# Optimization experiments

Measured on AMD Instinct MI355X. Metric: run time of the kernel, lower is better.

Reference implementation:

```python
import jax, jax.numpy as jnp
import numpy as np

N, E, D, H, C, L = 50000, 600000, 128, 128, 64, 3
LN_EPS = 1e-5


def setup_inputs() -> dict:
    key = jax.random.key(0)
    ks = jax.random.split(key, 6)
    x = jax.random.normal(ks[0], (N, D), jnp.float32)
    edge_index = jax.random.randint(ks[1], (2, E), 0, N, jnp.int32)
    Wg = jax.random.normal(ks[2], (L, D, H), jnp.float32) * (1.0 / np.sqrt(D))
    bg = jnp.zeros((L, H), jnp.float32)
    ln_g = jnp.ones((L, H), jnp.float32)
    ln_b = jnp.zeros((L, H), jnp.float32)
    mlp_W1 = jax.random.normal(ks[3], (D + L * H, H), jnp.float32) * (1.0 / np.sqrt(D + L * H))
    mlp_b1 = jnp.zeros((H,), jnp.float32)
    mlp_W2 = jax.random.normal(ks[4], (H, C), jnp.float32) * (1.0 / np.sqrt(H))
    mlp_b2 = jnp.zeros((C,), jnp.float32)
    return {"x": x, "edge_index": edge_index, "Wg": Wg, "bg": bg,
            "ln_g": ln_g, "ln_b": ln_b, "mlp_W1": mlp_W1, "mlp_b1": mlp_b1,
            "mlp_W2": mlp_W2, "mlp_b2": mlp_b2}


def _layer_norm(h, g, b):
    mu = jnp.mean(h, axis=-1, keepdims=True)
    var = jnp.mean((h - mu) ** 2, axis=-1, keepdims=True)
    return g * (h - mu) * jax.lax.rsqrt(var + LN_EPS) + b


def _gcn(h, W, b, src, dst, dinv):
    # GCNConv with added self-loops and symmetric normalization:
    # out = D^{-1/2} (A + I) D^{-1/2} (h W) + b
    hW = h @ W                                   # [N, H]
    coef = (dinv[src] * dinv[dst])[:, None]      # [E, 1]
    agg = jax.ops.segment_sum(hW[src] * coef, dst, num_segments=N)
    agg = agg + hW * (dinv * dinv)[:, None]      # self-loop term
    return agg + b


def reference(x, edge_index, Wg, bg, ln_g, ln_b, mlp_W1, mlp_b1, mlp_W2, mlp_b2):
    src, dst = edge_index[0], edge_index[1]
    # degree including self-loop
    deg = jnp.ones((N,), x.dtype).at[dst].add(1.0)
    dinv = jax.lax.rsqrt(deg)
    feats = [x]
    h = x
    for i in range(L):  # small fixed layer count
        h = _gcn(h, Wg[i], bg[i], src, dst, dinv)
        h = _layer_norm(h, ln_g[i], ln_b[i])
        h = jax.nn.relu(h)
        feats.append(h)
    xc = jnp.concatenate(feats, axis=1)          # [N, D + L*H]
    z = jax.nn.relu(xc @ mlp_W1 + mlp_b1)
    z = z @ mlp_W2 + mlp_b2
    return jax.nn.softmax(z, axis=1)
```

## Files before the change

### kernel.cpp

```cpp
#include <hip/hip_runtime.h>
#include <math.h>

#define D 128
#define HH 128
#define CC 64
#define NLAYERS 3
#define LN_EPS 1e-5f

typedef __attribute__((ext_vector_type(8))) short bf16x8;
typedef __attribute__((ext_vector_type(4))) float f32x4;
typedef unsigned short u16;
typedef unsigned int u32;

__device__ __forceinline__ u16 f2bf(float f) {
    u32 u = __float_as_uint(f);
    u32 r = u + 0x7FFFu + ((u >> 16) & 1u);
    return (u16)(r >> 16);
}
__device__ __forceinline__ float bf2f(u16 h) {
    return __uint_as_float(((u32)h) << 16);
}

__global__ void k_prep(const float* __restrict__ x, u16* __restrict__ xh,
                       const float* __restrict__ Wg, u16* __restrict__ WgtH,
                       const float* __restrict__ W1, u16* __restrict__ W1tH,
                       const float* __restrict__ W2, u16* __restrict__ W2tH,
                       u16* __restrict__ W2tL,
                       int* __restrict__ cnt, int N)
{
    int i = blockIdx.x * blockDim.x + threadIdx.x;
    if (i < N) { cnt[i] = 0; return; }
    i -= N;
    int nx4 = N * (D / 4);
    if (i < nx4) {
        float4 v = *(const float4*)(x + (size_t)i * 4);
        int row = i >> 5, c = (i & 31) << 2;
        ushort4 o;
        o.x = f2bf(v.x); o.y = f2bf(v.y); o.z = f2bf(v.z); o.w = f2bf(v.w);
        *(ushort4*)&xh[(size_t)row * 512 + c] = o;
        return;
    }
    i -= nx4;
    if (i < NLAYERS * D * HH) {
        int k = i >> 7, n = i & 127;
        int kc = k >> 5, q = (k >> 3) & 3, j = k & 7;
        WgtH[(((kc * 4 + q) << 7) + n) * 8 + j] = f2bf(Wg[i]);
        return;
    }
    i -= NLAYERS * D * HH;
    if (i < (D + NLAYERS * HH) * HH) {
        int k = i >> 7, n = i & 127;
        int kc = k >> 5, q = (k >> 3) & 3, j = k & 7;
        W1tH[(((kc * 4 + q) << 7) + n) * 8 + j] = f2bf(W1[i]);
        return;
    }
    i -= (D + NLAYERS * HH) * HH;
    if (i < HH * CC) {
        int k = i >> 6, n = i & 63;
        int kc = k >> 5, q = (k >> 3) & 3, j = k & 7;
        float v = W2[i];
        u16 h = f2bf(v);
        int o = (((kc * 4 + q) << 6) + n) * 8 + j;
        W2tH[o] = h;
        W2tL[o] = f2bf(v - bf2f(h));
    }
}


__global__ void k_count(const int* __restrict__ dst, int* __restrict__ cnt, int E) {
    int i = blockIdx.x * blockDim.x + threadIdx.x;
    if (i < E) atomicAdd(&cnt[dst[i]], 1);
}

__global__ void k_scan_a(const int* __restrict__ cnt, int* __restrict__ rowptr,
                         int* __restrict__ bsum, int N) {
    __shared__ int s[1024];
    int tid = threadIdx.x;
    int i = blockIdx.x * 1024 + tid;
    int v = (i < N) ? cnt[i] : 0;
    s[tid] = v;
    __syncthreads();
    for (int off = 1; off < 1024; off <<= 1) {
        int t = (tid >= off) ? s[tid - off] : 0;
        __syncthreads();
        s[tid] += t;
        __syncthreads();
    }
    if (i < N) rowptr[i] = s[tid] - v;
    if (tid == 1023) bsum[blockIdx.x] = s[tid];
}

__global__ void k_scan_c(int* __restrict__ rowptr, const int* __restrict__ bsum,
                         const int* __restrict__ cnt, float* __restrict__ dinv,
                         int* __restrict__ cursor, int N, int E, int nsb) {
    __shared__ int sb[64];
    if (threadIdx.x < 64) {
        int t = threadIdx.x;
        int v = (t < nsb) ? bsum[t] : 0;
        int incl = v;
        #pragma unroll
        for (int off = 1; off < 64; off <<= 1) {
            int u = __shfl_up(incl, off, 64);
            if (t >= off) incl += u;
        }
        sb[t] = incl - v;
    }
    __syncthreads();
    int i = blockIdx.x * blockDim.x + threadIdx.x;
    if (i < N) {
        int v = rowptr[i] + sb[i >> 10];
        rowptr[i] = v;
        cursor[i] = v;
        dinv[i] = rsqrtf(1.0f + (float)cnt[i]);
    }
    if (i == 0) rowptr[N] = E;
}

__global__ void k_scatter(const int* __restrict__ src, const int* __restrict__ dst,
                          const float* __restrict__ dinv,
                          int* __restrict__ cursor, int2* __restrict__ ecol, int E) {
    int i = blockIdx.x * blockDim.x + threadIdx.x;
    if (i < E) {
        int s = src[i], d = dst[i];
        int p = atomicAdd(&cursor[d], 1);
        float c = dinv[s] * dinv[d];
        ecol[p] = make_int2(s, __float_as_int(c));
    }
}

__global__ __launch_bounds__(256) void k_gemm_lf(
    const u16* __restrict__ A, int colOff,
    const u16* __restrict__ Bt, u16* __restrict__ OUTb, int N)
{
    const int tid  = threadIdx.x;
    const int lane = tid & 63;
    const int wave = tid >> 6;
    const int wr   = wave & 1;
    const int wc   = wave >> 1;
    const int quad = lane >> 4;
    const int l15  = lane & 15;
    const int row0 = blockIdx.x * 64;

    const u16* pA[2];
    #pragma unroll
    for (int i = 0; i < 2; ++i) {
        int r = row0 + wr * 32 + i * 16 + l15;
        if (r >= N) r = N - 1;
        pA[i] = A + (size_t)r * 512 + colOff + quad * 8;
    }
    const u16* pB = Bt + ((size_t)quad * 128 + wc * 64 + l15) * 8;

    bf16x8 ah[4][2], bh[4][4];
    #pragma unroll
    for (int kc = 0; kc < 4; ++kc) {
        #pragma unroll
        for (int i = 0; i < 2; ++i)
            ah[kc][i] = *(const bf16x8*)(pA[i] + kc * 32);
        #pragma unroll
        for (int j = 0; j < 4; ++j)
            bh[kc][j] = *(const bf16x8*)(pB + (size_t)kc * 4096 + j * 128);
    }

    f32x4 acc[2][4];
    #pragma unroll
    for (int i = 0; i < 2; ++i)
        #pragma unroll
        for (int j = 0; j < 4; ++j)
            #pragma unroll
            for (int r = 0; r < 4; ++r) acc[i][j][r] = 0.f;

    #pragma unroll
    for (int kc = 0; kc < 4; ++kc)
        #pragma unroll
        for (int i = 0; i < 2; ++i)
            #pragma unroll
            for (int j = 0; j < 4; ++j)
                acc[i][j] = __builtin_amdgcn_mfma_f32_16x16x32_bf16(ah[kc][i], bh[kc][j], acc[i][j], 0, 0, 0);

    #pragma unroll
    for (int i = 0; i < 2; ++i)
        #pragma unroll
        for (int j = 0; j < 4; ++j) {
            int col = wc * 64 + j * 16 + l15;
            #pragma unroll
            for (int r = 0; r < 4; ++r) {
                int grow = row0 + wr * 32 + i * 16 + quad * 4 + r;
                if (grow < N)
                    OUTb[(size_t)grow * 128 + col] = f2bf(acc[i][j][r]);
            }
        }
}

__global__ __launch_bounds__(256) void k_mlp_fused(
    const u16* __restrict__ xcH,
    const u16* __restrict__ B1t, const float* __restrict__ b1,
    const u16* __restrict__ W2h, const u16* __restrict__ W2l,
    const float* __restrict__ b2, float* __restrict__ out, int N)
{
    __shared__ float sAcc[32 * 132];
    __shared__ u16 sZh[32 * 128];
    __shared__ u16 sZl[32 * 128];

    const int tid  = threadIdx.x;
    const int lane = tid & 63;
    const int wave = tid >> 6;
    const int wc   = wave & 1;
    const int kg   = wave >> 1;
    const int quad = lane >> 4;
    const int l15  = lane & 15;
    const int row0 = blockIdx.x * 32;

    const u16* pA[2];
    #pragma unroll
    for (int f = 0; f < 2; ++f) {
        int r = row0 + f * 16 + l15;
        if (r >= N) r = N - 1;
        pA[f] = xcH + (size_t)r * 512 + quad * 8;
    }
    const u16* pB = B1t + ((size_t)quad * 128 + wc * 64 + l15) * 8;

    f32x4 acc[2][4];
    #pragma unroll
    for (int f = 0; f < 2; ++f)
        #pragma unroll
        for (int j = 0; j < 4; ++j)
            #pragma unroll
            for (int r = 0; r < 4; ++r) acc[f][j][r] = 0.f;

    bf16x8 abuf[3][2], bbuf[3][4];
    #define LOADI(t, s)                                                          \
        {                                                                        \
            const int g = kg * 8 + (t);                                          \
            _Pragma("unroll")                                                    \
            for (int f = 0; f < 2; ++f)                                          \
                abuf[s][f] = *(const bf16x8*)(pA[f] + g * 32);                   \
            _Pragma("unroll")                                                    \
            for (int j = 0; j < 4; ++j)                                          \
                bbuf[s][j] = *(const bf16x8*)(pB + (size_t)g * 4096 + j * 128);  \
        }
    LOADI(0, 0)
    LOADI(1, 1)
    #pragma unroll
    for (int t = 0; t < 8; ++t) {
        if (t + 2 < 8) {
            const int s = (t + 2) % 3;
            LOADI(t + 2, s)
        }
        const int u = t % 3;
        #pragma unroll
        for (int f = 0; f < 2; ++f)
            #pragma unroll
            for (int j = 0; j < 4; ++j)
                acc[f][j] = __builtin_amdgcn_mfma_f32_16x16x32_bf16(abuf[u][f], bbuf[u][j], acc[f][j], 0, 0, 0);
    }
    #undef LOADI

    if (kg == 1) {
        #pragma unroll
        for (int f = 0; f < 2; ++f)
            #pragma unroll
            for (int jt = 0; jt < 4; ++jt) {
                int col = wc * 64 + jt * 16 + l15;
                #pragma unroll
                for (int r = 0; r < 4; ++r) {
                    int row = f * 16 + quad * 4 + r;
                    sAcc[row * 132 + col] = acc[f][jt][r];
                }
            }
    }
    __syncthreads();
    if (kg == 0) {
        #pragma unroll
        for (int jt = 0; jt < 4; ++jt) {
            int col = wc * 64 + jt * 16 + l15;
            float bv = b1[col];
            int qq = col >> 3, jj = col & 7;
            #pragma unroll
            for (int f = 0; f < 2; ++f) {
                #pragma unroll
                for (int rr = 0; rr < 4; ++rr) {
                    int row = f * 16 + quad * 4 + rr;
                    float v = fmaxf(acc[f][jt][rr] + sAcc[row * 132 + col] + bv, 0.f);
                    u16 h = f2bf(v);
                    sZh[(qq * 32 + row) * 8 + jj] = h;
                    sZl[(qq * 32 + row) * 8 + jj] = f2bf(v - bf2f(h));
                }
            }
        }
    }
    __syncthreads();

    if (kg == 0) {
        f32x4 oacc[4];
        #pragma unroll
        for (int j = 0; j < 4; ++j)
            #pragma unroll
            for (int r = 0; r < 4; ++r) oacc[j][r] = 0.f;

        #pragma unroll
        for (int kc = 0; kc < 4; ++kc) {
            int qq = kc * 4 + quad;
            bf16x8 zh = *(const bf16x8*)&sZh[(qq * 32 + wc * 16 + l15) * 8];
            bf16x8 zl = *(const bf16x8*)&sZl[(qq * 32 + wc * 16 + l15) * 8];
            #pragma unroll
            for (int jt = 0; jt < 4; ++jt) {
                int n = jt * 16 + l15;
                bf16x8 wh = *(const bf16x8*)&W2h[(qq * 64 + n) * 8];
                bf16x8 wl = *(const bf16x8*)&W2l[(qq * 64 + n) * 8];
                oacc[jt] = __builtin_amdgcn_mfma_f32_16x16x32_bf16(zh, wh, oacc[jt], 0, 0, 0);
                oacc[jt] = __builtin_amdgcn_mfma_f32_16x16x32_bf16(zh, wl, oacc[jt], 0, 0, 0);
                oacc[jt] = __builtin_amdgcn_mfma_f32_16x16x32_bf16(zl, wh, oacc[jt], 0, 0, 0);
            }
        }

        #pragma unroll
        for (int jt = 0; jt < 4; ++jt) {
            float bv = b2[jt * 16 + l15];
            #pragma unroll
            for (int r = 0; r < 4; ++r) oacc[jt][r] += bv;
        }
        #pragma unroll
        for (int r = 0; r < 4; ++r) {
            float m = fmaxf(fmaxf(oacc[0][r], oacc[1][r]), fmaxf(oacc[2][r], oacc[3][r]));
            #pragma unroll
            for (int mask = 8; mask; mask >>= 1) m = fmaxf(m, __shfl_xor(m, mask, 64));
            float p0 = __expf(oacc[0][r] - m);
            float p1 = __expf(oacc[1][r] - m);
            float p2 = __expf(oacc[2][r] - m);
            float p3 = __expf(oacc[3][r] - m);
            float s = p0 + p1 + p2 + p3;
            #pragma unroll
            for (int mask = 8; mask; mask >>= 1) s += __shfl_xor(s, mask, 64);
            float inv = 1.0f / s;
            int grow = row0 + wc * 16 + quad * 4 + r;
            if (grow < N) {
                float* o = out + (size_t)grow * CC + l15;
                o[0]  = p0 * inv;
                o[16] = p1 * inv;
                o[32] = p2 * inv;
                o[48] = p3 * inv;
            }
        }
    }
}

__global__ __launch_bounds__(256, 8) void k_agg_ln(
    const u16* __restrict__ hWb,
    const int* __restrict__ rowptr, const int2* __restrict__ ecol,
    const float* __restrict__ dinv,
    const float* __restrict__ bg, const float* __restrict__ g,
    const float* __restrict__ b,
    u16* __restrict__ outHi, int N)
{
    const int lane = threadIdx.x & 63;
    const int h    = lane >> 5;
    const int c0   = (lane & 31) << 2;

    const float4 bgv = *(const float4*)(bg + c0);
    const float4 gv  = *(const float4*)(g + c0);
    const float4 bv  = *(const float4*)(b + c0);

    const int nwaves = gridDim.x * 4;
    for (int wid = blockIdx.x * 4 + (threadIdx.x >> 6); wid < N; wid += nwaves) {
        float di = dinv[wid];
        float sc = (h == 0) ? di * di : 0.f;

        uint2 hv = *(const uint2*)(hWb + (size_t)wid * HH + c0);
        float a0 = bf2f((u16)hv.x) * sc;
        float a1 = bf2f((u16)(hv.x >> 16)) * sc;
        float a2 = bf2f((u16)hv.y) * sc;
        float a3 = bf2f((u16)(hv.y >> 16)) * sc;
        float q0 = 0.f, q1 = 0.f, q2 = 0.f, q3 = 0.f;

        int e0 = rowptr[wid];
        int m  = rowptr[wid + 1] - e0;
        int ch = (m - h + 1) >> 1;
        const int2* ep = ecol + e0 + h;

        int k = 0;
        for (; k + 4 <= ch; k += 4) {
            int2 p[4];
            uint2 v[4];
            #pragma unroll
            for (int t = 0; t < 4; ++t) p[t] = ep[2 * (k + t)];
            #pragma unroll
            for (int t = 0; t < 4; ++t)
                v[t] = *(const uint2*)(hWb + (size_t)p[t].x * HH + c0);
            #pragma unroll
            for (int t = 0; t < 4; ++t) {
                float c = __int_as_float(p[t].y);
                float x0 = bf2f((u16)v[t].x) * c;
                float x1 = bf2f((u16)(v[t].x >> 16)) * c;
                float x2 = bf2f((u16)v[t].y) * c;
                float x3 = bf2f((u16)(v[t].y >> 16)) * c;
                if (t & 1) { q0 += x0; q1 += x1; q2 += x2; q3 += x3; }
                else       { a0 += x0; a1 += x1; a2 += x2; a3 += x3; }
            }
        }
        for (; k < ch; ++k) {
            int2 p = ep[2 * k];
            uint2 v = *(const uint2*)(hWb + (size_t)p.x * HH + c0);
            float c = __int_as_float(p.y);
            a0 += bf2f((u16)v.x) * c;
            a1 += bf2f((u16)(v.x >> 16)) * c;
            a2 += bf2f((u16)v.y) * c;
            a3 += bf2f((u16)(v.y >> 16)) * c;
        }
        a0 += q0; a1 += q1; a2 += q2; a3 += q3;

        a0 += __shfl_xor(a0, 32, 64);
        a1 += __shfl_xor(a1, 32, 64);
        a2 += __shfl_xor(a2, 32, 64);
        a3 += __shfl_xor(a3, 32, 64);
        a0 += bgv.x; a1 += bgv.y; a2 += bgv.z; a3 += bgv.w;

        float ssum = (a0 + a1) + (a2 + a3);
        #pragma unroll
        for (int off = 16; off; off >>= 1) ssum += __shfl_xor(ssum, off, 64);
        float mu = ssum * (1.0f / 128.0f);
        float d0 = a0 - mu, d1 = a1 - mu, d2 = a2 - mu, d3 = a3 - mu;
        float vsum = (d0 * d0 + d1 * d1) + (d2 * d2 + d3 * d3);
        #pragma unroll
        for (int off = 16; off; off >>= 1) vsum += __shfl_xor(vsum, off, 64);
        float rstd = rsqrtf(vsum * (1.0f / 128.0f) + LN_EPS);

        if (!h) {
            float o0 = fmaxf(gv.x * d0 * rstd + bv.x, 0.f);
            float o1 = fmaxf(gv.y * d1 * rstd + bv.y, 0.f);
            float o2 = fmaxf(gv.z * d2 * rstd + bv.z, 0.f);
            float o3 = fmaxf(gv.w * d3 * rstd + bv.w, 0.f);
            uint2 o;
            o.x = (u32)f2bf(o0) | ((u32)f2bf(o1) << 16);
            o.y = (u32)f2bf(o2) | ((u32)f2bf(o3) << 16);
            *(uint2*)&outHi[(size_t)wid * 512 + c0] = o;
        }
    }
}

extern "C" void kernel_launch(void* const* d_in, const int* in_sizes, int n_in,
                              void* d_out, int out_size, void* d_ws, size_t ws_size,
                              hipStream_t stream) {
    const float* x   = (const float*)d_in[0];
    const int*   ei  = (const int*)  d_in[1];
    const float* Wg  = (const float*)d_in[2];
    const float* bg  = (const float*)d_in[3];
    const float* lng = (const float*)d_in[4];
    const float* lnb = (const float*)d_in[5];
    const float* W1  = (const float*)d_in[6];
    const float* b1  = (const float*)d_in[7];
    const float* W2  = (const float*)d_in[8];
    const float* b2  = (const float*)d_in[9];
    float* out = (float*)d_out;

    const int N = in_sizes[0] / D;
    const int E = in_sizes[1] / 2;
    const int* srcp = ei;
    const int* dstp = ei + E;

    char* ws = (char*)d_ws;
    size_t off = 0;
    auto alloc = [&](size_t bytes) -> void* {
        void* p = ws + off;
        off += (bytes + 511) & ~(size_t)511;
        return p;
    };
    int*   cnt    = (int*)  alloc((size_t)N * 4);
    int*   rowptr = (int*)  alloc((size_t)(N + 1) * 4);
    int*   cursor = (int*)  alloc((size_t)N * 4);
    int*   bsum   = (int*)  alloc(64 * 4);
    int2*  ecol   = (int2*) alloc((size_t)E * 8);
    float* dinv   = (float*)alloc((size_t)N * 4);
    u16*   hWb    = (u16*)  alloc((size_t)N * HH * 2);
    u16*   xcH    = (u16*)  alloc((size_t)N * 512 * 2);
    u16*   WgtH   = (u16*)  alloc((size_t)NLAYERS * D * HH * 2);
    u16*   W1tH   = (u16*)  alloc((size_t)(D + NLAYERS * HH) * HH * 2);
    u16*   W2tH   = (u16*)  alloc((size_t)HH * CC * 2);
    u16*   W2tL   = (u16*)  alloc((size_t)HH * CC * 2);

    const int B = 256;
    const int gE = (E + B - 1) / B;
    const int nsb = (N + 1023) / 1024;

    const int prepTotal = N + N * (D / 4) + NLAYERS * D * HH
                        + (D + NLAYERS * HH) * HH + HH * CC;
    k_prep<<<(prepTotal + B - 1) / B, B, 0, stream>>>(x, xcH, Wg, WgtH, W1, W1tH,
                                                      W2, W2tH, W2tL, cnt, N);
    k_count<<<gE, B, 0, stream>>>(dstp, cnt, E);
    k_scan_a<<<nsb, 1024, 0, stream>>>(cnt, rowptr, bsum, N);
    k_scan_c<<<(N + B - 1) / B, B, 0, stream>>>(rowptr, bsum, cnt, dinv, cursor, N, E, nsb);
    k_scatter<<<gE, B, 0, stream>>>(srcp, dstp, dinv, cursor, ecol, E);

    const int gemmBlocks = (N + 63) / 64;
    const int mlpBlocks  = (N + 31) / 32;
    const int aggBlocks  = 2048;

    for (int l = 0; l < NLAYERS; ++l) {
        k_gemm_lf<<<gemmBlocks, B, 0, stream>>>(xcH, l * HH,
                                                WgtH + (size_t)l * D * HH, hWb, N);
        k_agg_ln<<<aggBlocks, B, 0, stream>>>(hWb, rowptr, ecol, dinv,
                                              bg + (size_t)l * HH,
                                              lng + (size_t)l * HH,
                                              lnb + (size_t)l * HH,
                                              xcH + (size_t)(l + 1) * HH, N);
    }

    k_mlp_fused<<<mlpBlocks, B, 0, stream>>>(xcH, W1tH, b1,
                                             W2tH, W2tL, b2, out, N);
}
```

Before: 321.7 us.

## Split aggregation wave into four edge streams with 16-byte row gathers

The aggregation+LayerNorm kernel now splits each 64-lane wave into four groups of 16 lanes. Each group handles every fourth edge and loads 8 bf16 features per lane with 16-byte loads, where before two halves each loaded 4 features. This gives more independent gathers in flight per node and wider memory transactions, at the cost of more cross-lane reductions and a lower unroll depth per edge stream. The block scan is also rewritten to use wavefront shuffles instead of a barrier-heavy shared-memory Hillis-Steele loop.

```diff
diff --git a/kernel.cpp b/kernel.cpp
--- a/kernel.cpp
+++ b/kernel.cpp
@@ -74,20 +74,32 @@
 
 __global__ void k_scan_a(const int* __restrict__ cnt, int* __restrict__ rowptr,
                          int* __restrict__ bsum, int N) {
-    __shared__ int s[1024];
-    int tid = threadIdx.x;
+    __shared__ int ws[16];
+    int tid  = threadIdx.x;
+    int lane = tid & 63, wv = tid >> 6;
     int i = blockIdx.x * 1024 + tid;
     int v = (i < N) ? cnt[i] : 0;
-    s[tid] = v;
+    int incl = v;
+    #pragma unroll
+    for (int off = 1; off < 64; off <<= 1) {
+        int u = __shfl_up(incl, off, 64);
+        if (lane >= off) incl += u;
+    }
+    if (lane == 63) ws[wv] = incl;
     __syncthreads();
-    for (int off = 1; off < 1024; off <<= 1) {
-        int t = (tid >= off) ? s[tid - off] : 0;
-        __syncthreads();
-        s[tid] += t;
-        __syncthreads();
-    }
-    if (i < N) rowptr[i] = s[tid] - v;
-    if (tid == 1023) bsum[blockIdx.x] = s[tid];
+    if (wv == 0) {
+        int s = (lane < 16) ? ws[lane] : 0;
+        #pragma unroll
+        for (int off = 1; off < 16; off <<= 1) {
+            int u = __shfl_up(s, off, 64);
+            if (lane >= off) s += u;
+        }
+        if (lane < 16) ws[lane] = s;
+    }
+    __syncthreads();
+    int add = (wv == 0) ? 0 : ws[wv - 1];
+    if (i < N) rowptr[i] = add + incl - v;
+    if (tid == 1023) bsum[blockIdx.x] = ws[15];
 }
 
 __global__ void k_scan_c(int* __restrict__ rowptr, const int* __restrict__ bsum,
@@ -353,86 +365,98 @@
     u16* __restrict__ outHi, int N)
 {
     const int lane = threadIdx.x & 63;
-    const int h    = lane >> 5;
-    const int c0   = (lane & 31) << 2;
-
-    const float4 bgv = *(const float4*)(bg + c0);
-    const float4 gv  = *(const float4*)(g + c0);
-    const float4 bv  = *(const float4*)(b + c0);
+    const int qd   = lane >> 4;
+    const int c0   = (lane & 15) << 3;
+
+    const float4 bgA = *(const float4*)(bg + c0);
+    const float4 bgB = *(const float4*)(bg + c0 + 4);
 
     const int nwaves = gridDim.x * 4;
     for (int wid = blockIdx.x * 4 + (threadIdx.x >> 6); wid < N; wid += nwaves) {
         float di = dinv[wid];
-        float sc = (h == 0) ? di * di : 0.f;
-
-        uint2 hv = *(const uint2*)(hWb + (size_t)wid * HH + c0);
-        float a0 = bf2f((u16)hv.x) * sc;
-        float a1 = bf2f((u16)(hv.x >> 16)) * sc;
-        float a2 = bf2f((u16)hv.y) * sc;
-        float a3 = bf2f((u16)(hv.y >> 16)) * sc;
-        float q0 = 0.f, q1 = 0.f, q2 = 0.f, q3 = 0.f;
+        float sc = (qd == 0) ? di * di : 0.f;
+
+        uint4 hv = *(const uint4*)(hWb + (size_t)wid * HH + c0);
+        float a0 = bf2f((u16)hv.x) * sc, a1 = bf2f((u16)(hv.x >> 16)) * sc;
+        float a2 = bf2f((u16)hv.y) * sc, a3 = bf2f((u16)(hv.y >> 16)) * sc;
+        float a4 = bf2f((u16)hv.z) * sc, a5 = bf2f((u16)(hv.z >> 16)) * sc;
+        float a6 = bf2f((u16)hv.w) * sc, a7 = bf2f((u16)(hv.w >> 16)) * sc;
 
         int e0 = rowptr[wid];
         int m  = rowptr[wid + 1] - e0;
-        int ch = (m - h + 1) >> 1;
-        const int2* ep = ecol + e0 + h;
+        int cq = (m - qd + 3) >> 2;
+        const int2* ep = ecol + e0 + qd;
 
         int k = 0;
-        for (; k + 4 <= ch; k += 4) {
+        for (; k + 4 <= cq; k += 4) {
             int2 p[4];
-            uint2 v[4];
-            #pragma unroll
-            for (int t = 0; t < 4; ++t) p[t] = ep[2 * (k + t)];
+            uint4 v[4];
+            #pragma unroll
+            for (int t = 0; t < 4; ++t) p[t] = ep[4 * (k + t)];
             #pragma unroll
             for (int t = 0; t < 4; ++t)
-                v[t] = *(const uint2*)(hWb + (size_t)p[t].x * HH + c0);
+                v[t] = *(const uint4*)(hWb + (size_t)p[t].x * HH + c0);
             #pragma unroll
             for (int t = 0; t < 4; ++t) {
                 float c = __int_as_float(p[t].y);
-                float x0 = bf2f((u16)v[t].x) * c;
-                float x1 = bf2f((u16)(v[t].x >> 16)) * c;
-                float x2 = bf2f((u16)v[t].y) * c;
-                float x3 = bf2f((u16)(v[t].y >> 16)) * c;
-                if (t & 1) { q0 += x0; q1 += x1; q2 += x2; q3 += x3; }
-                else       { a0 += x0; a1 += x1; a2 += x2; a3 += x3; }
+                a0 += bf2f((u16)v[t].x) * c;  a1 += bf2f((u16)(v[t].x >> 16)) * c;
+                a2 += bf2f((u16)v[t].y) * c;  a3 += bf2f((u16)(v[t].y >> 16)) * c;
+                a4 += bf2f((u16)v[t].z) * c;  a5 += bf2f((u16)(v[t].z >> 16)) * c;
+                a6 += bf2f((u16)v[t].w) * c;  a7 += bf2f((u16)(v[t].w >> 16)) * c;
             }
         }
-        for (; k < ch; ++k) {
-            int2 p = ep[2 * k];
-            uint2 v = *(const uint2*)(hWb + (size_t)p.x * HH + c0);
+        for (; k < cq; ++k) {
+            int2 p = ep[4 * k];
+            uint4 v = *(const uint4*)(hWb + (size_t)p.x * HH + c0);
             float c = __int_as_float(p.y);
-            a0 += bf2f((u16)v.x) * c;
-            a1 += bf2f((u16)(v.x >> 16)) * c;
-            a2 += bf2f((u16)v.y) * c;
-            a3 += bf2f((u16)(v.y >> 16)) * c;
-        }
-        a0 += q0; a1 += q1; a2 += q2; a3 += q3;
-
-        a0 += __shfl_xor(a0, 32, 64);
-        a1 += __shfl_xor(a1, 32, 64);
-        a2 += __shfl_xor(a2, 32, 64);
-        a3 += __shfl_xor(a3, 32, 64);
-        a0 += bgv.x; a1 += bgv.y; a2 += bgv.z; a3 += bgv.w;
-
-        float ssum = (a0 + a1) + (a2 + a3);
-        #pragma unroll
-        for (int off = 16; off; off >>= 1) ssum += __shfl_xor(ssum, off, 64);
+            a0 += bf2f((u16)v.x) * c;  a1 += bf2f((u16)(v.x >> 16)) * c;
+            a2 += bf2f((u16)v.y) * c;  a3 += bf2f((u16)(v.y >> 16)) * c;
+            a4 += bf2f((u16)v.z) * c;  a5 += bf2f((u16)(v.z >> 16)) * c;
+            a6 += bf2f((u16)v.w) * c;  a7 += bf2f((u16)(v.w >> 16)) * c;
+        }
+
+        a0 += __shfl_xor(a0, 16, 64); a0 += __shfl_xor(a0, 32, 64);
+        a1 += __shfl_xor(a1, 16, 64); a1 += __shfl_xor(a1, 32, 64);
+        a2 += __shfl_xor(a2, 16, 64); a2 += __shfl_xor(a2, 32, 64);
+        a3 += __shfl_xor(a3, 16, 64); a3 += __shfl_xor(a3, 32, 64);
+        a4 += __shfl_xor(a4, 16, 64); a4 += __shfl_xor(a4, 32, 64);
+        a5 += __shfl_xor(a5, 16, 64); a5 += __shfl_xor(a5, 32, 64);
+        a6 += __shfl_xor(a6, 16, 64); a6 += __shfl_xor(a6, 32, 64);
+        a7 += __shfl_xor(a7, 16, 64); a7 += __shfl_xor(a7, 32, 64);
+        a0 += bgA.x; a1 += bgA.y; a2 += bgA.z; a3 += bgA.w;
+        a4 += bgB.x; a5 += bgB.y; a6 += bgB.z; a7 += bgB.w;
+
+        float ssum = ((a0 + a1) + (a2 + a3)) + ((a4 + a5) + (a6 + a7));
+        #pragma unroll
+        for (int off = 8; off; off >>= 1) ssum += __shfl_xor(ssum, off, 64);
         float mu = ssum * (1.0f / 128.0f);
         float d0 = a0 - mu, d1 = a1 - mu, d2 = a2 - mu, d3 = a3 - mu;
-        float vsum = (d0 * d0 + d1 * d1) + (d2 * d2 + d3 * d3);
-        #pragma unroll
-        for (int off = 16; off; off >>= 1) vsum += __shfl_xor(vsum, off, 64);
+        float d4 = a4 - mu, d5 = a5 - mu, d6 = a6 - mu, d7 = a7 - mu;
+        float vsum = ((d0 * d0 + d1 * d1) + (d2 * d2 + d3 * d3))
+                   + ((d4 * d4 + d5 * d5) + (d6 * d6 + d7 * d7));
+        #pragma unroll
+        for (int off = 8; off; off >>= 1) vsum += __shfl_xor(vsum, off, 64);
         float rstd = rsqrtf(vsum * (1.0f / 128.0f) + LN_EPS);
 
-        if (!h) {
-            float o0 = fmaxf(gv.x * d0 * rstd + bv.x, 0.f);
-            float o1 = fmaxf(gv.y * d1 * rstd + bv.y, 0.f);
-            float o2 = fmaxf(gv.z * d2 * rstd + bv.z, 0.f);
-            float o3 = fmaxf(gv.w * d3 * rstd + bv.w, 0.f);
-            uint2 o;
+        if (qd == 0) {
+            const float4 gA = *(const float4*)(g + c0);
+            const float4 gB = *(const float4*)(g + c0 + 4);
+            const float4 bA = *(const float4*)(b + c0);
+            const float4 bB = *(const float4*)(b + c0 + 4);
+            float o0 = fmaxf(gA.x * d0 * rstd + bA.x, 0.f);
+            float o1 = fmaxf(gA.y * d1 * rstd + bA.y, 0.f);
+            float o2 = fmaxf(gA.z * d2 * rstd + bA.z, 0.f);
+            float o3 = fmaxf(gA.w * d3 * rstd + bA.w, 0.f);
+            float o4 = fmaxf(gB.x * d4 * rstd + bB.x, 0.f);
+            float o5 = fmaxf(gB.y * d5 * rstd + bB.y, 0.f);
+            float o6 = fmaxf(gB.z * d6 * rstd + bB.z, 0.f);
+            float o7 = fmaxf(gB.w * d7 * rstd + bB.w, 0.f);
+            uint4 o;
             o.x = (u32)f2bf(o0) | ((u32)f2bf(o1) << 16);
             o.y = (u32)f2bf(o2) | ((u32)f2bf(o3) << 16);
-            *(uint2*)&outHi[(size_t)wid * 512 + c0] = o;
+            o.z = (u32)f2bf(o4) | ((u32)f2bf(o5) << 16);
+            o.w = (u32)f2bf(o6) | ((u32)f2bf(o7) << 16);
+            *(uint4*)&outHi[(size_t)wid * 512 + c0] = o;
         }
     }
 }
```

Measured after the change: 376.3 us. 1.17x slower.

## Map one node per half-wave in aggregation and use wave-shuffle block scan

Applied to the files above, without the earlier changes.

The aggregation kernel now assigns one node to each 32-lane half-wave instead of splitting one node's edges across two half-waves. This removes the cross-half reduction and the idle output half, and handles the edge tail with a predicated three-edge batch. The scan kernel swaps its shared-memory Hillis-Steele loop, which needed many barriers, for wave shuffle scans plus a 16-entry shared fixup. The cost is that each half-wave walks a whole edge list serially, so latency per node grows and the two nodes in a wave can diverge when their degrees differ.

```diff
diff --git a/kernel.cpp b/kernel.cpp
--- a/kernel.cpp
+++ b/kernel.cpp
@@ -74,20 +74,32 @@
 
 __global__ void k_scan_a(const int* __restrict__ cnt, int* __restrict__ rowptr,
                          int* __restrict__ bsum, int N) {
-    __shared__ int s[1024];
-    int tid = threadIdx.x;
+    __shared__ int ws[16];
+    int tid  = threadIdx.x;
+    int lane = tid & 63, wv = tid >> 6;
     int i = blockIdx.x * 1024 + tid;
     int v = (i < N) ? cnt[i] : 0;
-    s[tid] = v;
+    int incl = v;
+    #pragma unroll
+    for (int off = 1; off < 64; off <<= 1) {
+        int u = __shfl_up(incl, off, 64);
+        if (lane >= off) incl += u;
+    }
+    if (lane == 63) ws[wv] = incl;
     __syncthreads();
-    for (int off = 1; off < 1024; off <<= 1) {
-        int t = (tid >= off) ? s[tid - off] : 0;
-        __syncthreads();
-        s[tid] += t;
-        __syncthreads();
-    }
-    if (i < N) rowptr[i] = s[tid] - v;
-    if (tid == 1023) bsum[blockIdx.x] = s[tid];
+    if (wv == 0) {
+        int s = (lane < 16) ? ws[lane] : 0;
+        #pragma unroll
+        for (int off = 1; off < 16; off <<= 1) {
+            int u = __shfl_up(s, off, 64);
+            if (lane >= off) s += u;
+        }
+        if (lane < 16) ws[lane] = s;
+    }
+    __syncthreads();
+    int add = (wv == 0) ? 0 : ws[wv - 1];
+    if (i < N) rowptr[i] = add + incl - v;
+    if (tid == 1023) bsum[blockIdx.x] = ws[15];
 }
 
 __global__ void k_scan_c(int* __restrict__ rowptr, const int* __restrict__ bsum,
@@ -353,17 +365,17 @@
     u16* __restrict__ outHi, int N)
 {
     const int lane = threadIdx.x & 63;
-    const int h    = lane >> 5;
     const int c0   = (lane & 31) << 2;
 
     const float4 bgv = *(const float4*)(bg + c0);
     const float4 gv  = *(const float4*)(g + c0);
     const float4 bv  = *(const float4*)(b + c0);
 
-    const int nwaves = gridDim.x * 4;
-    for (int wid = blockIdx.x * 4 + (threadIdx.x >> 6); wid < N; wid += nwaves) {
+    const int nslots = gridDim.x * 8;
+    for (int wid = blockIdx.x * 8 + ((threadIdx.x >> 6) << 1) + (lane >> 5);
+         wid < N; wid += nslots) {
         float di = dinv[wid];
-        float sc = (h == 0) ? di * di : 0.f;
+        float sc = di * di;
 
         uint2 hv = *(const uint2*)(hWb + (size_t)wid * HH + c0);
         float a0 = bf2f((u16)hv.x) * sc;
@@ -374,15 +386,14 @@
 
         int e0 = rowptr[wid];
         int m  = rowptr[wid + 1] - e0;
-        int ch = (m - h + 1) >> 1;
-        const int2* ep = ecol + e0 + h;
+        const int2* ep = ecol + e0;
 
         int k = 0;
-        for (; k + 4 <= ch; k += 4) {
+        for (; k + 4 <= m; k += 4) {
             int2 p[4];
             uint2 v[4];
             #pragma unroll
-            for (int t = 0; t < 4; ++t) p[t] = ep[2 * (k + t)];
+            for (int t = 0; t < 4; ++t) p[t] = ep[k + t];
             #pragma unroll
             for (int t = 0; t < 4; ++t)
                 v[t] = *(const uint2*)(hWb + (size_t)p[t].x * HH + c0);
@@ -397,21 +408,24 @@
                 else       { a0 += x0; a1 += x1; a2 += x2; a3 += x3; }
             }
         }
-        for (; k < ch; ++k) {
-            int2 p = ep[2 * k];
-            uint2 v = *(const uint2*)(hWb + (size_t)p.x * HH + c0);
-            float c = __int_as_float(p.y);
-            a0 += bf2f((u16)v.x) * c;
-            a1 += bf2f((u16)(v.x >> 16)) * c;
-            a2 += bf2f((u16)v.y) * c;
-            a3 += bf2f((u16)(v.y >> 16)) * c;
+        if (k < m) {
+            int2 p0 = ep[k];
+            int2 p1 = (k + 1 < m) ? ep[k + 1] : p0;
+            int2 p2 = (k + 2 < m) ? ep[k + 2] : p0;
+            uint2 v0 = *(const uint2*)(hWb + (size_t)p0.x * HH + c0);
+            uint2 v1 = *(const uint2*)(hWb + (size_t)p1.x * HH + c0);
+            uint2 v2 = *(const uint2*)(hWb + (size_t)p2.x * HH + c0);
+            float cc0 = __int_as_float(p0.y);
+            float cc1 = (k + 1 < m) ? __int_as_float(p1.y) : 0.f;
+            float cc2 = (k + 2 < m) ? __int_as_float(p2.y) : 0.f;
+            a0 += bf2f((u16)v0.x) * cc0;  a1 += bf2f((u16)(v0.x >> 16)) * cc0;
+            a2 += bf2f((u16)v0.y) * cc0;  a3 += bf2f((u16)(v0.y >> 16)) * cc0;
+            q0 += bf2f((u16)v1.x) * cc1;  q1 += bf2f((u16)(v1.x >> 16)) * cc1;
+            q2 += bf2f((u16)v1.y) * cc1;  q3 += bf2f((u16)(v1.y >> 16)) * cc1;
+            a0 += bf2f((u16)v2.x) * cc2;  a1 += bf2f((u16)(v2.x >> 16)) * cc2;
+            a2 += bf2f((u16)v2.y) * cc2;  a3 += bf2f((u16)(v2.y >> 16)) * cc2;
         }
         a0 += q0; a1 += q1; a2 += q2; a3 += q3;
-
-        a0 += __shfl_xor(a0, 32, 64);
-        a1 += __shfl_xor(a1, 32, 64);
-        a2 += __shfl_xor(a2, 32, 64);
-        a3 += __shfl_xor(a3, 32, 64);
         a0 += bgv.x; a1 += bgv.y; a2 += bgv.z; a3 += bgv.w;
 
         float ssum = (a0 + a1) + (a2 + a3);
@@ -424,16 +438,14 @@
         for (int off = 16; off; off >>= 1) vsum += __shfl_xor(vsum, off, 64);
         float rstd = rsqrtf(vsum * (1.0f / 128.0f) + LN_EPS);
 
-        if (!h) {
-            float o0 = fmaxf(gv.x * d0 * rstd + bv.x, 0.f);
-            float o1 = fmaxf(gv.y * d1 * rstd + bv.y, 0.f);
-            float o2 = fmaxf(gv.z * d2 * rstd + bv.z, 0.f);
-            float o3 = fmaxf(gv.w * d3 * rstd + bv.w, 0.f);
-            uint2 o;
-            o.x = (u32)f2bf(o0) | ((u32)f2bf(o1) << 16);
-            o.y = (u32)f2bf(o2) | ((u32)f2bf(o3) << 16);
-            *(uint2*)&outHi[(size_t)wid * 512 + c0] = o;
-        }
+        float o0 = fmaxf(gv.x * d0 * rstd + bv.x, 0.f);
+        float o1 = fmaxf(gv.y * d1 * rstd + bv.y, 0.f);
+        float o2 = fmaxf(gv.z * d2 * rstd + bv.z, 0.f);
+        float o3 = fmaxf(gv.w * d3 * rstd + bv.w, 0.f);
+        uint2 o;
+        o.x = (u32)f2bf(o0) | ((u32)f2bf(o1) << 16);
+        o.y = (u32)f2bf(o2) | ((u32)f2bf(o3) << 16);
+        *(uint2*)&outHi[(size_t)wid * 512 + c0] = o;
     }
 }
 
```

Measured after the change: 304.6 us. 5.3% less time.
